# Optimization experiments

Hardware: AMD Instinct MI355X
Metric: run time of the kernel (lower is better)

The kernel has to match this reference:

```python
import jax, jax.numpy as jnp
import numpy as np
from jax import lax


def _bilinear_gather(img, ys, xs):
    """img: [B,H,W,C]; ys,xs: [B,K,H,W] fractional coords. Zero padding outside.
    Returns [B,K,H,W,C]."""
    B, H, W, C = img.shape
    y0 = jnp.floor(ys)
    x0 = jnp.floor(xs)
    wy = (ys - y0)[..., None]
    wx = (xs - x0)[..., None]
    y0i = y0.astype(jnp.int32)
    x0i = x0.astype(jnp.int32)
    flat = img.reshape(B, H * W, C)

    def gather(yi, xi):
        valid = (yi >= 0) & (yi < H) & (xi >= 0) & (xi < W)
        yc = jnp.clip(yi, 0, H - 1)
        xc = jnp.clip(xi, 0, W - 1)
        idx = (yc * W + xc).reshape(B, -1, 1)
        g = jnp.take_along_axis(flat, idx, axis=1).reshape(yi.shape + (C,))
        return g * valid[..., None].astype(img.dtype)

    v00 = gather(y0i, x0i)
    v01 = gather(y0i, x0i + 1)
    v10 = gather(y0i + 1, x0i)
    v11 = gather(y0i + 1, x0i + 1)
    one = jnp.asarray(1.0, img.dtype)
    return (v00 * (one - wy) * (one - wx) + v01 * (one - wy) * wx
            + v10 * wy * (one - wx) + v11 * wy * wx)


def _forward(x, w_off, b_off, w_def, b_def, w_attn, b_attn):
    B, Cin, H, W = x.shape
    Cout = w_def.shape[0]
    # offset conv: 3x3, pad 1 -> [B, 18, H, W]
    off = lax.conv_general_dilated(x, w_off, (1, 1), ((1, 1), (1, 1)))
    off = off + b_off[None, :, None, None]
    off = off.reshape(B, 9, 2, H, W)
    dy = off[:, :, 0]  # [B,9,H,W], torchvision order: (dy, dx) per kernel pt
    dx = off[:, :, 1]
    # kernel point grid, row-major over (kh, kw)
    ky, kx = jnp.meshgrid(jnp.arange(3), jnp.arange(3), indexing='ij')
    ky = ky.reshape(9).astype(x.dtype)
    kx = kx.reshape(9).astype(x.dtype)
    ii = jnp.arange(H, dtype=x.dtype)
    jj = jnp.arange(W, dtype=x.dtype)
    # sample position = (out_pos - pad + k) + offset, pad=1, stride=1
    ys = ii[None, None, :, None] - 1.0 + ky[None, :, None, None] + dy
    xs = jj[None, None, None, :] - 1.0 + kx[None, :, None, None] + dx
    img = x.transpose(0, 2, 3, 1)  # [B,H,W,Cin]
    sampled = _bilinear_gather(img, ys, xs)  # [B,9,H,W,Cin]
    wk = w_def.reshape(Cout, Cin, 9)  # row-major kernel pts match ky/kx
    out = jnp.einsum('bkhwc,ock->bohw', sampled, wk) + b_def[None, :, None, None]
    # spatial attention: 1x1 conv -> sigmoid gate
    attn = jnp.einsum('bchw,oc->bohw', out, w_attn[:, :, 0, 0]) + b_attn[None, :, None, None]
    out = out * jax.nn.sigmoid(attn)
    return jax.nn.relu(out)


def setup_inputs() -> dict:
    key = jax.random.key(0)
    ks = jax.random.split(key, 5)
    B, C, H, W = 4, 128, 128, 128
    x = jax.random.normal(ks[0], (B, C, H, W), dtype=jnp.float32)
    w_off = jax.random.normal(ks[1], (18, C, 3, 3), dtype=jnp.float32) * 0.02
    b_off = jnp.zeros((18,), dtype=jnp.float32)
    w_def = jax.random.normal(ks[2], (C, C, 3, 3), dtype=jnp.float32) * (1.0 / np.sqrt(C * 9))
    b_def = jnp.zeros((C,), dtype=jnp.float32)
    w_attn = jax.random.normal(ks[3], (1, C, 1, 1), dtype=jnp.float32) * (1.0 / np.sqrt(C))
    b_attn = jnp.zeros((1,), dtype=jnp.float32)
    return {"x": x, "w_off": w_off, "b_off": b_off, "w_def": w_def,
            "b_def": b_def, "w_attn": w_attn, "b_attn": b_attn}


def reference(x, w_off, b_off, w_def, b_def, w_attn, b_attn):
    return _forward(x, w_off, b_off, w_def, b_def, w_attn, b_attn)
```

## Files before the change

### kernel.cpp

```cpp
#include <hip/hip_runtime.h>
#include <math.h>

#define Cch 128
#define Hh 128
#define Ww 128
#define HW (Hh * Ww)

typedef __attribute__((ext_vector_type(8))) short short8;
typedef __attribute__((ext_vector_type(4))) float float4v;
typedef __attribute__((ext_vector_type(2))) float float2v;
typedef __attribute__((ext_vector_type(4))) unsigned int uint4v;

__device__ __forceinline__ unsigned short f2bf(float f) {
    unsigned u = __float_as_uint(f);
    return (unsigned short)((u + 0x8000u) >> 16);
}
__device__ __forceinline__ float2v up2(unsigned u) {
    return (float2v){__uint_as_float(u << 16), __uint_as_float(u & 0xffff0000u)};
}
__device__ __forceinline__ unsigned packbf2(float lo, float hi) {
    unsigned a = __float_as_uint(lo), b = __float_as_uint(hi);
    return ((a + 0x8000u) >> 16) | ((b + 0x8000u) & 0xffff0000u);
}

__global__ __launch_bounds__(256) void transpose_x_bf16(const float* __restrict__ x,
                                                        unsigned short* __restrict__ xt) {
    __shared__ float tile[32][33];
    int b  = blockIdx.z;
    int c0 = blockIdx.y * 32;
    int p0 = blockIdx.x * 32;
    int tx = threadIdx.x, ty = threadIdx.y;
    const float* xb = x + (size_t)b * Cch * HW;
    unsigned short* xtb = xt + (size_t)b * HW * Cch;
    #pragma unroll
    for (int i = 0; i < 32; i += 8)
        tile[ty + i][tx] = __builtin_nontemporal_load(&xb[(size_t)(c0 + ty + i) * HW + p0 + tx]);
    __syncthreads();
    #pragma unroll
    for (int i = 0; i < 32; i += 8)
        xtb[(size_t)(p0 + ty + i) * Cch + c0 + tx] = f2bf(tile[tx][ty + i]);
}

#define NFB (9 * 4 * 8 * 64 * 8)
#define NFO (9 * 4 * 2 * 64 * 8)
__global__ __launch_bounds__(256) void build_frags(const float* __restrict__ w_def,
                                                   const float* __restrict__ w_off,
                                                   unsigned short* __restrict__ wfB,
                                                   unsigned short* __restrict__ wfO) {
    int idx = blockIdx.x * 256 + threadIdx.x;
    if (idx < NFB) {
        int j = idx & 7, lane = (idx >> 3) & 63, t = (idx >> 9) & 7;
        int q = (idx >> 12) & 3, k = idx >> 14;
        int c = 32 * q + 8 * (lane >> 4) + j;
        int o = 16 * t + (lane & 15);
        wfB[idx] = f2bf(w_def[(size_t)(o * Cch + c) * 9 + k]);
    } else if (idx < NFB + NFO) {
        int i2 = idx - NFB;
        int j = i2 & 7, lane = (i2 >> 3) & 63, t = (i2 >> 9) & 1;
        int q = (i2 >> 10) & 3, k = i2 >> 12;
        int c = 32 * q + 8 * (lane >> 4) + j;
        int o = 16 * t + (lane & 15);
        wfO[i2] = (o < 18) ? f2bf(w_off[(size_t)(o * Cch + c) * 9 + k]) : (unsigned short)0;
    }
}

__device__ __forceinline__ void blk_map(int blk, int& b, int& h, int& w0) {
    int xcd = blk & 7;
    b = xcd >> 1;
    int seg = ((xcd & 1) << 8) | (blk >> 3);
    h  = seg >> 2;
    w0 = (seg & 3) << 5;
}

__global__ __launch_bounds__(128, 2) void fused_srt(const unsigned short* __restrict__ xt,
                                                    const unsigned short* __restrict__ wfB,
                                                    const unsigned short* __restrict__ wfO,
                                                    const float* __restrict__ b_off,
                                                    const float* __restrict__ b_def,
                                                    const float* __restrict__ w_attn,
                                                    const float* __restrict__ b_attn,
                                                    float* __restrict__ out) {
    __shared__ float4v red[2 * 8 * 64];
    __shared__ float   offs[32 * 18];
    __shared__ uint4v  smw[2 * 4 * 64];
    int b, h, w0;
    blk_map(blockIdx.x, b, h, w0);
    int tid  = threadIdx.x;
    int wave = tid >> 6;
    int lane = tid & 63;
    int col  = lane & 15;
    int s    = lane >> 4;
    int spx  = lane >> 2;
    int sch  = lane & 3;
    int cbase = 64 * wave;
    int csrt  = cbase + sch * 8;
    int wbase = wave * 256;
    int rIdx  = wbase + ((lane & 15) * 4 + (lane >> 4));

    const unsigned short* xtb = xt + (size_t)b * HW * Cch;

    {
        float4v acc2[2][2];
        #pragma unroll
        for (int pt = 0; pt < 2; ++pt)
            #pragma unroll
            for (int t = 0; t < 2; ++t) {
                int o = 16 * t + col;
                float bv = (wave == 0 && o < 18) ? b_off[o] : 0.0f;
                acc2[pt][t] = (float4v){bv, bv, bv, bv};
            }

        #pragma unroll
        for (int k = 0; k < 9; ++k) {
            int y = h + (k / 3) - 1;
            bool vy = (y >= 0) && (y < Hh);
            int yc = min(max(y, 0), Hh - 1);
            int dxk = (k % 3) - 1;
            int  ofs[2];
            bool val[2];
            #pragma unroll
            for (int pt = 0; pt < 2; ++pt) {
                int px = w0 + 16 * pt + spx;
                int xs = px + dxk;
                val[pt] = vy && (xs >= 0) && (xs < Ww);
                int xc  = min(max(xs, 0), Ww - 1);
                ofs[pt] = (yc * Ww + xc) * Cch + csrt;
            }
            #pragma unroll
            for (int pt = 0; pt < 2; ++pt)
                #pragma unroll
                for (int qq = 0; qq < 2; ++qq) {
                    uint4v av = *(const uint4v*)(xtb + ofs[pt] + 32 * qq);
                    if (!val[pt]) av = (uint4v){0u, 0u, 0u, 0u};
                    smw[wbase + (pt * 2 + qq) * 64 + lane] = av;
                }
            short8 aa[2][2];
            #pragma unroll
            for (int pt = 0; pt < 2; ++pt)
                #pragma unroll
                for (int qq = 0; qq < 2; ++qq)
                    aa[pt][qq] = __builtin_bit_cast(short8, smw[rIdx + (pt * 2 + qq) * 64]);
            #pragma unroll
            for (int qq = 0; qq < 2; ++qq) {
                int q = 2 * wave + qq;
                #pragma unroll
                for (int t = 0; t < 2; ++t) {
                    short8 bv = *(const short8*)(wfO + ((size_t)((k * 4 + q) * 2 + t) * 64 + lane) * 8);
                    #pragma unroll
                    for (int pt = 0; pt < 2; ++pt)
                        acc2[pt][t] = __builtin_amdgcn_mfma_f32_16x16x32_bf16(aa[pt][qq], bv, acc2[pt][t], 0, 0, 0);
                }
            }
        }
        if (wave == 1) {
            #pragma unroll
            for (int pt = 0; pt < 2; ++pt)
                #pragma unroll
                for (int t = 0; t < 2; ++t)
                    red[(pt * 2 + t) * 64 + lane] = acc2[pt][t];
        }
        __syncthreads();
        if (wave == 0) {
            #pragma unroll
            for (int pt = 0; pt < 2; ++pt)
                #pragma unroll
                for (int t = 0; t < 2; ++t) {
                    float4v v = acc2[pt][t] + red[(pt * 2 + t) * 64 + lane];
                    int o = 16 * t + col;
                    if (o < 18) {
                        #pragma unroll
                        for (int r = 0; r < 4; ++r)
                            offs[(16 * pt + 4 * s + r) * 18 + o] = v[r];
                    }
                }
        }
        __syncthreads();
    }

    float4v acc[2][8];
    #pragma unroll
    for (int pt = 0; pt < 2; ++pt)
        #pragma unroll
        for (int t = 0; t < 8; ++t) {
            float bv = (wave == 0) ? b_def[16 * t + col] : 0.0f;
            acc[pt][t] = (float4v){bv, bv, bv, bv};
        }

    int    oaddr[2][4];
    float  wxy[2][4];
    uint4v u[2][8];

#define CALC_TAP(K_) do {                                                    \
    int ky = ((K_) * 11) >> 5;                                               \
    int kx = (K_) - 3 * ky;                                                  \
    _Pragma("unroll")                                                        \
    for (int pt = 0; pt < 2; ++pt) {                                         \
        int pxl = 16 * pt + spx;                                             \
        int px  = w0 + pxl;                                                  \
        float2 dv = *(const float2*)&offs[pxl * 18 + 2 * (K_)];              \
        float ys = (float)(h - 1 + ky) + dv.x;                               \
        float xs = (float)(px - 1 + kx) + dv.y;                              \
        float y0f = floorf(ys), x0f = floorf(xs);                            \
        float wy = ys - y0f, wx = xs - x0f;                                  \
        int y0 = (int)y0f, x0 = (int)x0f;                                    \
        bool vy0 = (y0 >= 0) && (y0 < Hh);                                   \
        bool vy1 = (y0 + 1 >= 0) && (y0 + 1 < Hh);                           \
        bool vx0 = (x0 >= 0) && (x0 < Ww);                                   \
        bool vx1 = (x0 + 1 >= 0) && (x0 + 1 < Ww);                           \
        int y0c = min(max(y0, 0), Hh - 1), y1c = min(max(y0 + 1, 0), Hh - 1);\
        int x0c = min(max(x0, 0), Ww - 1), x1c = min(max(x0 + 1, 0), Ww - 1);\
        wxy[pt][0] = vx0 ? (1.0f - wx) : 0.0f;                               \
        wxy[pt][1] = vx1 ? wx : 0.0f;                                        \
        wxy[pt][2] = vy0 ? (1.0f - wy) : 0.0f;                               \
        wxy[pt][3] = vy1 ? wy : 0.0f;                                        \
        oaddr[pt][0] = (y0c * Ww + x0c) * Cch + csrt;                        \
        oaddr[pt][1] = (y0c * Ww + x1c) * Cch + csrt;                        \
        oaddr[pt][2] = (y1c * Ww + x0c) * Cch + csrt;                        \
        oaddr[pt][3] = (y1c * Ww + x1c) * Cch + csrt;                        \
    }                                                                        \
} while (0)

#define LOAD_TAP() do {                                                      \
    _Pragma("unroll")                                                        \
    for (int pt = 0; pt < 2; ++pt)                                           \
        _Pragma("unroll")                                                    \
        for (int qq = 0; qq < 2; ++qq)                                       \
            _Pragma("unroll")                                                \
            for (int c4 = 0; c4 < 4; ++c4)                                   \
                u[pt][qq * 4 + c4] =                                         \
                    *(const uint4v*)(xtb + oaddr[pt][c4] + 32 * qq);         \
} while (0)

    CALC_TAP(0);
    LOAD_TAP();

    #pragma unroll
    for (int k = 0; k < 9; ++k) {
        const unsigned short* wk = wfB + (size_t)k * 16384 + (size_t)(2 * wave) * 4096;
        short8 bva[8], bvb[8];
        #pragma unroll
        for (int t = 0; t < 8; ++t) {
            bva[t] = *(const short8*)(wk + (size_t)t * 512 + (size_t)lane * 8);
            bvb[t] = *(const short8*)(wk + 4096 + (size_t)t * 512 + (size_t)lane * 8);
        }
        #pragma unroll
        for (int pt = 0; pt < 2; ++pt) {
            float2v A0 = (float2v){wxy[pt][0], wxy[pt][0]};
            float2v A1 = (float2v){wxy[pt][1], wxy[pt][1]};
            float2v B0 = (float2v){wxy[pt][2], wxy[pt][2]};
            float2v B1 = (float2v){wxy[pt][3], wxy[pt][3]};
            #pragma unroll
            for (int qq = 0; qq < 2; ++qq) {
                uint4v res;
                #pragma unroll
                for (int j = 0; j < 4; ++j) {
                    float2v p00 = up2(u[pt][qq * 4 + 0][j]);
                    float2v p01 = up2(u[pt][qq * 4 + 1][j]);
                    float2v p10 = up2(u[pt][qq * 4 + 2][j]);
                    float2v p11 = up2(u[pt][qq * 4 + 3][j]);
                    float2v t0 = __builtin_elementwise_fma(A1, p01, A0 * p00);
                    float2v t1 = __builtin_elementwise_fma(A1, p11, A0 * p10);
                    float2v rr = __builtin_elementwise_fma(B1, t1, B0 * t0);
                    res[j] = packbf2(rr.x, rr.y);
                }
                smw[wbase + (pt * 2 + qq) * 64 + lane] = res;
            }
        }
        if (k < 8) {
            CALC_TAP(k + 1);
            LOAD_TAP();
        }
        short8 afr[2][2];
        #pragma unroll
        for (int pt = 0; pt < 2; ++pt)
            #pragma unroll
            for (int qq = 0; qq < 2; ++qq)
                afr[pt][qq] = __builtin_bit_cast(short8, smw[rIdx + (pt * 2 + qq) * 64]);
        #pragma unroll
        for (int t = 0; t < 8; ++t) {
            acc[0][t] = __builtin_amdgcn_mfma_f32_16x16x32_bf16(afr[0][0], bva[t], acc[0][t], 0, 0, 0);
            acc[1][t] = __builtin_amdgcn_mfma_f32_16x16x32_bf16(afr[1][0], bva[t], acc[1][t], 0, 0, 0);
        }
        #pragma unroll
        for (int t = 0; t < 8; ++t) {
            acc[0][t] = __builtin_amdgcn_mfma_f32_16x16x32_bf16(afr[0][1], bvb[t], acc[0][t], 0, 0, 0);
            acc[1][t] = __builtin_amdgcn_mfma_f32_16x16x32_bf16(afr[1][1], bvb[t], acc[1][t], 0, 0, 0);
        }
    }
#undef CALC_TAP
#undef LOAD_TAP

    if (wave == 1) {
        #pragma unroll
        for (int pt = 0; pt < 2; ++pt)
            #pragma unroll
            for (int t = 0; t < 8; ++t)
                red[(pt * 8 + t) * 64 + lane] = acc[pt][t];
    }
    __syncthreads();
    if (wave == 0) {
        #pragma unroll
        for (int pt = 0; pt < 2; ++pt)
            #pragma unroll
            for (int t = 0; t < 8; ++t)
                acc[pt][t] += red[(pt * 8 + t) * 64 + lane];

        float wA[8];
        #pragma unroll
        for (int t = 0; t < 8; ++t) wA[t] = w_attn[16 * t + col];
        float battn = b_attn[0];
        #pragma unroll
        for (int pt = 0; pt < 2; ++pt) {
            float sig[4];
            #pragma unroll
            for (int r = 0; r < 4; ++r) {
                float pr = 0.0f;
                #pragma unroll
                for (int t = 0; t < 8; ++t) pr = fmaf(acc[pt][t][r], wA[t], pr);
                #pragma unroll
                for (int m = 1; m < 16; m <<= 1) pr += __shfl_xor(pr, m, 64);
                sig[r] = 1.0f / (1.0f + expf(-(pr + battn)));
            }
            #pragma unroll
            for (int t = 0; t < 8; ++t) {
                int o = 16 * t + col;
                float4v v;
                #pragma unroll
                for (int r = 0; r < 4; ++r)
                    v[r] = fmaxf(acc[pt][t][r] * sig[r], 0.0f);
                float* dst = out + ((size_t)(b * Cch + o)) * HW + h * Ww + w0 + 16 * pt + 4 * s;
                __builtin_nontemporal_store(v, (float4v*)dst);
            }
        }
    }
}

extern "C" void kernel_launch(void* const* d_in, const int* in_sizes, int n_in,
                              void* d_out, int out_size, void* d_ws, size_t ws_size,
                              hipStream_t stream) {
    const float* x      = (const float*)d_in[0];
    const float* w_off  = (const float*)d_in[1];
    const float* b_off  = (const float*)d_in[2];
    const float* w_def  = (const float*)d_in[3];
    const float* b_def  = (const float*)d_in[4];
    const float* w_attn = (const float*)d_in[5];
    const float* b_attn = (const float*)d_in[6];
    float* out = (float*)d_out;

    char* ws = (char*)d_ws;
    unsigned short* xt  = (unsigned short*)ws;
    unsigned short* wfB = (unsigned short*)(ws + 16777216);
    unsigned short* wfO = (unsigned short*)(ws + 17072128);

    transpose_x_bf16<<<dim3(512, 4, 4), dim3(32, 8), 0, stream>>>(x, xt);
    build_frags<<<720, 256, 0, stream>>>(w_def, w_off, wfB, wfO);
    fused_srt<<<2048, 128, 0, stream>>>(xt, wfB, wfO, b_off, b_def, w_attn, b_attn, out);
}
```

Measured before the change: 157.9 us.

## Vectorize bf16 transpose-pack, raise MFMA wave priority, use regular output stores

The NCHW-to-NHWC bf16 pack kernel is rewritten to load float4 pairs of channels, pack them into bf16x2 words in shared memory and write 16-byte vectors. The old kernel did scalar loads and 2-byte stores. s_setprio raises wave priority around the MFMA blocks in both the offset and main loops so matrix work is issued ahead of other waves. The final output stores switch from nontemporal to ordinary stores. Together these aim to cut pre-processing bandwidth waste and improve issue interleaving, at the risk of LDS bank conflicts in the new 64x68 tile.

```diff
diff --git a/kernel.cpp b/kernel.cpp
--- a/kernel.cpp
+++ b/kernel.cpp
@@ -23,22 +23,37 @@
     return ((a + 0x8000u) >> 16) | ((b + 0x8000u) & 0xffff0000u);
 }
 
-__global__ __launch_bounds__(256) void transpose_x_bf16(const float* __restrict__ x,
-                                                        unsigned short* __restrict__ xt) {
-    __shared__ float tile[32][33];
-    int b  = blockIdx.z;
-    int c0 = blockIdx.y * 32;
-    int p0 = blockIdx.x * 32;
-    int tx = threadIdx.x, ty = threadIdx.y;
-    const float* xb = x + (size_t)b * Cch * HW;
-    unsigned short* xtb = xt + (size_t)b * HW * Cch;
+__global__ __launch_bounds__(256) void pack_x_v3(const float* __restrict__ x,
+                                                 unsigned short* __restrict__ xt) {
+    __shared__ unsigned int tile[64][68];
+    int t   = threadIdx.x;
+    int blk = blockIdx.x;
+    int b   = blk >> 8;
+    int p0  = (blk & 255) << 6;
+    const float* xb = x + (size_t)b * Cch * HW + p0;
+
+    int c2i = t >> 4;
+    int q   = t & 15;
     #pragma unroll
-    for (int i = 0; i < 32; i += 8)
-        tile[ty + i][tx] = __builtin_nontemporal_load(&xb[(size_t)(c0 + ty + i) * HW + p0 + tx]);
+    for (int it = 0; it < 4; ++it) {
+        int c2 = it * 16 + c2i;
+        int px = q * 4;
+        float4v a = *(const float4v*)&xb[(size_t)(2 * c2) * HW + px];
+        float4v c = *(const float4v*)&xb[(size_t)(2 * c2 + 1) * HW + px];
+        #pragma unroll
+        for (int j = 0; j < 4; ++j)
+            tile[px + j][c2] = packbf2(a[j], c[j]);
+    }
     __syncthreads();
+    unsigned short* xtb = xt + (size_t)b * HW * Cch + (size_t)p0 * Cch;
+    int g  = t & 15;
+    int pw = t >> 4;
     #pragma unroll
-    for (int i = 0; i < 32; i += 8)
-        xtb[(size_t)(p0 + ty + i) * Cch + c0 + tx] = f2bf(tile[tx][ty + i]);
+    for (int it = 0; it < 4; ++it) {
+        int p = pw + 16 * it;
+        uint4v v = *(const uint4v*)&tile[p][g * 4];
+        *(uint4v*)(xtb + (size_t)p * Cch + g * 8) = v;
+    }
 }
 
 #define NFB (9 * 4 * 8 * 64 * 8)
@@ -140,6 +155,7 @@
                 #pragma unroll
                 for (int qq = 0; qq < 2; ++qq)
                     aa[pt][qq] = __builtin_bit_cast(short8, smw[rIdx + (pt * 2 + qq) * 64]);
+            __builtin_amdgcn_s_setprio(1);
             #pragma unroll
             for (int qq = 0; qq < 2; ++qq) {
                 int q = 2 * wave + qq;
@@ -151,6 +167,7 @@
                         acc2[pt][t] = __builtin_amdgcn_mfma_f32_16x16x32_bf16(aa[pt][qq], bv, acc2[pt][t], 0, 0, 0);
                 }
             }
+            __builtin_amdgcn_s_setprio(0);
         }
         if (wave == 1) {
             #pragma unroll
@@ -210,7 +227,7 @@
         int y0c = min(max(y0, 0), Hh - 1), y1c = min(max(y0 + 1, 0), Hh - 1);\
         int x0c = min(max(x0, 0), Ww - 1), x1c = min(max(x0 + 1, 0), Ww - 1);\
         wxy[pt][0] = vx0 ? (1.0f - wx) : 0.0f;                               \
-        wxy[pt][1] = vx1 ? wx : 0.0f;                                        \
+        wxy[pt][1] = vx1 ? wx : 0.0f;                               \
         wxy[pt][2] = vy0 ? (1.0f - wy) : 0.0f;                               \
         wxy[pt][3] = vy1 ? wy : 0.0f;                                        \
         oaddr[pt][0] = (y0c * Ww + x0c) * Cch + csrt;                        \
@@ -276,6 +293,7 @@
             #pragma unroll
             for (int qq = 0; qq < 2; ++qq)
                 afr[pt][qq] = __builtin_bit_cast(short8, smw[rIdx + (pt * 2 + qq) * 64]);
+        __builtin_amdgcn_s_setprio(1);
         #pragma unroll
         for (int t = 0; t < 8; ++t) {
             acc[0][t] = __builtin_amdgcn_mfma_f32_16x16x32_bf16(afr[0][0], bva[t], acc[0][t], 0, 0, 0);
@@ -286,6 +304,7 @@
             acc[0][t] = __builtin_amdgcn_mfma_f32_16x16x32_bf16(afr[0][1], bvb[t], acc[0][t], 0, 0, 0);
             acc[1][t] = __builtin_amdgcn_mfma_f32_16x16x32_bf16(afr[1][1], bvb[t], acc[1][t], 0, 0, 0);
         }
+        __builtin_amdgcn_s_setprio(0);
     }
 #undef CALC_TAP
 #undef LOAD_TAP
@@ -329,7 +348,7 @@
                 for (int r = 0; r < 4; ++r)
                     v[r] = fmaxf(acc[pt][t][r] * sig[r], 0.0f);
                 float* dst = out + ((size_t)(b * Cch + o)) * HW + h * Ww + w0 + 16 * pt + 4 * s;
-                __builtin_nontemporal_store(v, (float4v*)dst);
+                *(float4v*)dst = v;
             }
         }
     }
@@ -352,7 +371,7 @@
     unsigned short* wfB = (unsigned short*)(ws + 16777216);
     unsigned short* wfO = (unsigned short*)(ws + 17072128);
 
-    transpose_x_bf16<<<dim3(512, 4, 4), dim3(32, 8), 0, stream>>>(x, xt);
+    pack_x_v3<<<1024, 256, 0, stream>>>(x, xt);
     build_frags<<<720, 256, 0, stream>>>(w_def, w_off, wfB, wfO);
     fused_srt<<<2048, 128, 0, stream>>>(xt, wfB, wfO, b_off, b_def, w_attn, b_attn, out);
 }
```

Result: slower. 163.8 us (+3.8%).
